# Kernel tuning notes

Measured on AMD Instinct MI355X. Metric: run time of the kernel, lower is better.

Reference implementation:

```python
import jax, jax.numpy as jnp
import numpy as np

N_RAYS, N_SAMPLES, HIDDEN, N_VOXELS = 8192, 256, 64, 1000


def setup_inputs() -> dict:
    key = jax.random.key(0)
    ks = jax.random.split(key, 10)
    ray_start = jax.random.normal(ks[0], (N_RAYS, 3), jnp.float32)
    ray_dir = jax.random.normal(ks[1], (N_RAYS, 3), jnp.float32)
    ray_dir = ray_dir / jnp.linalg.norm(ray_dir, axis=-1, keepdims=True)
    # monotonically increasing depths along each ray
    sampled_depth = jnp.sort(jax.random.uniform(ks[2], (N_RAYS, N_SAMPLES), jnp.float32) * 4.0 + 0.5, axis=-1)
    sampled_dists = jax.random.uniform(ks[3], (N_RAYS, N_SAMPLES), jnp.float32) * 0.02 + 1e-3
    sampled_idx = jax.random.randint(ks[4], (N_RAYS, N_SAMPLES), -333, N_VOXELS).astype(jnp.int64)
    W1 = jax.random.normal(ks[5], (3, HIDDEN), jnp.float32) * 0.5
    b1 = jnp.zeros((HIDDEN,), jnp.float32)
    w_sigma = jax.random.normal(ks[6], (HIDDEN,), jnp.float32) * 0.5
    W_rgb = jax.random.normal(ks[7], (HIDDEN, 3), jnp.float32) * 0.5
    W_dir = jax.random.normal(ks[8], (3, 3), jnp.float32) * 0.5
    b_rgb = jnp.zeros((3,), jnp.float32)
    return {"ray_start": ray_start, "ray_dir": ray_dir, "sampled_depth": sampled_depth,
            "sampled_dists": sampled_dists, "sampled_idx": sampled_idx,
            "W1": W1, "b1": b1, "w_sigma": w_sigma, "W_rgb": W_rgb, "W_dir": W_dir, "b_rgb": b_rgb}


def _volume_render(ray_start, ray_dir, sampled_depth, sampled_dists, sampled_idx,
                   W1, b1, w_sigma, W_rgb, W_dir, b_rgb):
    # sampled_xyz = ray(ray_start, ray_dir, depth)
    xyz = ray_start[:, None, :] + ray_dir[:, None, :] * sampled_depth[..., None]  # [N,P,3]
    h = jax.nn.relu(jnp.einsum('npi,ih->nph', xyz, W1) + b1)                      # [N,P,H]
    sigma = jnp.einsum('nph,h->np', h, w_sigma)                                   # [N,P]
    rgb = jax.nn.sigmoid(jnp.einsum('nph,hc->npc', h, W_rgb)
                         + jnp.einsum('ni,ic->nc', ray_dir, W_dir)[:, None, :] + b_rgb)  # [N,P,3]
    mask = (sampled_idx != -1).astype(sigma.dtype)                                # [N,P]
    # free_energy = relu(sigma) * dists * 7.0, scattered back with zeros at misses
    free_energy = jax.nn.relu(sigma) * sampled_dists * 7.0 * mask
    shifted = jnp.concatenate([jnp.zeros_like(free_energy[:, :1]), free_energy[:, :-1]], axis=-1)
    a = 1.0 - jnp.exp(-free_energy)
    b = jnp.exp(-jnp.cumsum(shifted, axis=-1))
    probs = a * b                                                                 # [N,P]
    depths = jnp.sum(sampled_depth * probs, axis=-1)                              # [N]
    missed = 1.0 - jnp.sum(probs, axis=-1)                                        # [N]
    colors = jnp.sum(rgb * probs[..., None], axis=-2)                             # [N,3]
    return jnp.concatenate([colors, depths[:, None], missed[:, None], probs], axis=-1)  # [N, 3+1+1+P]


def reference(ray_start, ray_dir, sampled_depth, sampled_dists, sampled_idx,
              W1, b1, w_sigma, W_rgb, W_dir, b_rgb):
    return _volume_render(ray_start, ray_dir, sampled_depth, sampled_dists, sampled_idx,
                          W1, b1, w_sigma, W_rgb, W_dir, b_rgb)
```

## Files before the change

kernel.cpp:

```cpp
#include <hip/hip_runtime.h>

#define NRAYS 8192
#define NS    256
#define HID   64
#define NPAIR 32
#define RPB   8
#define SPT   8

typedef _Float16 f16x2 __attribute__((ext_vector_type(2)));

static __device__ __forceinline__ float fdot2(f16x2 a, f16x2 b, float c) {
    return __builtin_amdgcn_fdot2(a, b, c, false);
}
static __device__ __forceinline__ f16x2 mk2(float a, float b) {
    f16x2 v; v.x = (_Float16)a; v.y = (_Float16)b; return v;
}

struct __align__(16) W4  { f16x2 ws, wr, wg, wb; };
struct __align__(8)  AB2 { f16x2 A, B; };

__global__ __launch_bounds__(256) void vr_kernel(
    const float* __restrict__ ray_start,
    const float* __restrict__ ray_dir,
    const float* __restrict__ sampled_depth,
    const float* __restrict__ sampled_dists,
    const int*   __restrict__ sampled_idx,
    const float* __restrict__ W1,
    const float* __restrict__ b1,
    const float* __restrict__ w_sigma,
    const float* __restrict__ W_rgb,
    const float* __restrict__ W_dir,
    const float* __restrict__ b_rgb,
    float* __restrict__ out)
{
    __shared__ W4  sW[NPAIR];
    __shared__ AB2 sAB[RPB][NPAIR];

    const int t = threadIdx.x;
    if (t < NPAIR) {
        const int h0 = 2*t, h1 = 2*t + 1;
        W4 w;
        w.ws = mk2(w_sigma[h0],    w_sigma[h1]);
        w.wr = mk2(W_rgb[h0*3+0],  W_rgb[h1*3+0]);
        w.wg = mk2(W_rgb[h0*3+1],  W_rgb[h1*3+1]);
        w.wb = mk2(W_rgb[h0*3+2],  W_rgb[h1*3+2]);
        sW[t] = w;
    }
    {
        const int rr  = t >> 5;
        const int k   = t & (NPAIR - 1);
        const int ray = blockIdx.x * RPB + rr;
        const float ox = ray_start[ray*3+0], oy = ray_start[ray*3+1], oz = ray_start[ray*3+2];
        const float dx = ray_dir[ray*3+0],  dy = ray_dir[ray*3+1],  dz = ray_dir[ray*3+2];
        const int h0 = 2*k, h1 = 2*k + 1;
        const float u0 = W1[h0], u1 = W1[HID + h0], u2 = W1[2*HID + h0];
        const float v0 = W1[h1], v1 = W1[HID + h1], v2 = W1[2*HID + h1];
        const float A0 = fmaf(u0, ox, fmaf(u1, oy, fmaf(u2, oz, b1[h0])));
        const float B0 = fmaf(u0, dx, fmaf(u1, dy, u2 * dz));
        const float A1 = fmaf(v0, ox, fmaf(v1, oy, fmaf(v2, oz, b1[h1])));
        const float B1 = fmaf(v0, dx, fmaf(v1, dy, v2 * dz));
        AB2 e; e.A = mk2(A0, A1); e.B = mk2(B0, B1);
        sAB[rr][k] = e;
    }
    __syncthreads();

    const int lane = t & 63;
    const int wave = t >> 6;
    const int hl   = lane & 31;
    const int r    = wave * 2 + (lane >> 5);
    const int ray  = blockIdx.x * RPB + r;

    const float dx = ray_dir[ray*3+0], dy = ray_dir[ray*3+1], dz = ray_dir[ray*3+2];
    const float dwr = fmaf(dx, W_dir[0], fmaf(dy, W_dir[3], fmaf(dz, W_dir[6], b_rgb[0])));
    const float dwg = fmaf(dx, W_dir[1], fmaf(dy, W_dir[4], fmaf(dz, W_dir[7], b_rgb[1])));
    const float dwb = fmaf(dx, W_dir[2], fmaf(dy, W_dir[5], fmaf(dz, W_dir[8], b_rgb[2])));

    const size_t rbase = (size_t)ray * NS + (size_t)hl * SPT;
    const float4 dep0 = ((const float4*)(sampled_depth + rbase))[0];
    const float4 dep1 = ((const float4*)(sampled_depth + rbase))[1];
    const float4 dst0 = ((const float4*)(sampled_dists + rbase))[0];
    const float4 dst1 = ((const float4*)(sampled_dists + rbase))[1];
    const int4   vi0  = ((const int4*)(sampled_idx + rbase))[0];
    const int4   vi1  = ((const int4*)(sampled_idx + rbase))[1];

    const float dpt[SPT] = {dep0.x, dep0.y, dep0.z, dep0.w, dep1.x, dep1.y, dep1.z, dep1.w};
    const float dsv[SPT] = {dst0.x, dst0.y, dst0.z, dst0.w, dst1.x, dst1.y, dst1.z, dst1.w};
    const int   vid[SPT] = {vi0.x, vi0.y, vi0.z, vi0.w, vi1.x, vi1.y, vi1.z, vi1.w};

    f16x2 d2[SPT];
#pragma unroll
    for (int j = 0; j < SPT; ++j) d2[j] = mk2(dpt[j], dpt[j]);
    const f16x2 zero2 = mk2(0.f, 0.f);

    float sig[SPT] = {0,0,0,0,0,0,0,0};
    float cr[SPT]  = {0,0,0,0,0,0,0,0};
    float cg[SPT]  = {0,0,0,0,0,0,0,0};
    float cb[SPT]  = {0,0,0,0,0,0,0,0};

#pragma unroll 4
    for (int k = 0; k < NPAIR; ++k) {
        const W4  w  = sW[k];
        const AB2 ab = sAB[r][k];
#pragma unroll
        for (int j = 0; j < SPT; ++j) {
            f16x2 hv = __builtin_elementwise_fma(ab.B, d2[j], ab.A);
            hv = __builtin_elementwise_max(hv, zero2);
            sig[j] = fdot2(hv, w.ws, sig[j]);
            cr[j]  = fdot2(hv, w.wr, cr[j]);
            cg[j]  = fdot2(hv, w.wg, cg[j]);
            cb[j]  = fdot2(hv, w.wb, cb[j]);
        }
    }

    float c[SPT];
    float run = 0.f;
#pragma unroll
    for (int j = 0; j < SPT; ++j) {
        float f = fmaxf(sig[j], 0.f) * dsv[j] * 7.0f;
        if (vid[j] == -1) f = 0.f;
        run += f;
        c[j] = run;
    }

    float tot = run;
#pragma unroll
    for (int off = 1; off < 32; off <<= 1) {
        const float v = __shfl_up(tot, off, 32);
        if (hl >= off) tot += v;
    }
    const float base = tot - run;

    float Eprev = __expf(-base);
    float prob[SPT];
    float s0 = 0.f, s1 = 0.f, s2 = 0.f, s3 = 0.f, s4 = 0.f;
#pragma unroll
    for (int j = 0; j < SPT; ++j) {
        const float Ej = __expf(-(base + c[j]));
        const float p  = Eprev - Ej;
        Eprev = Ej;
        prob[j] = p;
        const float rr = __builtin_amdgcn_rcpf(1.f + __expf(-(cr[j] + dwr)));
        const float gg = __builtin_amdgcn_rcpf(1.f + __expf(-(cg[j] + dwg)));
        const float bb = __builtin_amdgcn_rcpf(1.f + __expf(-(cb[j] + dwb)));
        s0 += p;
        s1 = fmaf(dpt[j], p, s1);
        s2 = fmaf(rr, p, s2);
        s3 = fmaf(gg, p, s3);
        s4 = fmaf(bb, p, s4);
    }

#pragma unroll
    for (int off = 16; off >= 1; off >>= 1) {
        s0 += __shfl_xor(s0, off, 32);
        s1 += __shfl_xor(s1, off, 32);
        s2 += __shfl_xor(s2, off, 32);
        s3 += __shfl_xor(s3, off, 32);
        s4 += __shfl_xor(s4, off, 32);
    }

    float* orow = out + (size_t)ray * (NS + 5);
#pragma unroll
    for (int j = 0; j < SPT; ++j)
        orow[5 + SPT*hl + j] = prob[j];

    if (hl == 0) {
        orow[0] = s2;
        orow[1] = s3;
        orow[2] = s4;
        orow[3] = s1;
        orow[4] = 1.f - s0;
    }
}

extern "C" void kernel_launch(void* const* d_in, const int* in_sizes, int n_in,
                              void* d_out, int out_size, void* d_ws, size_t ws_size,
                              hipStream_t stream)
{
    vr_kernel<<<NRAYS / RPB, 256, 0, stream>>>(
        (const float*)d_in[0],
        (const float*)d_in[1],
        (const float*)d_in[2],
        (const float*)d_in[3],
        (const int*)  d_in[4],
        (const float*)d_in[5],
        (const float*)d_in[6],
        (const float*)d_in[7],
        (const float*)d_in[8],
        (const float*)d_in[9],
        (const float*)d_in[10],
        (float*)d_out);
}
```

Measured before the change: 104.0 us.

## Map one ray per wave with four samples per lane

Each wave of 64 lanes now handles one ray, with four samples per lane, where before each half-wave handled a ray at eight samples per lane. Blocks hold four rays and the launch bound asks for eight blocks per CU. The per-ray hidden-layer coefficients are packed four units at a time into 16-byte shared entries, so each iteration does one shared load of A/B and two of weights. The aim is lower register pressure, higher occupancy and more threads overall. The cost is twice as many weight loads from shared memory per sample and longer 64-wide scan and reduction shuffle chains.

```diff
diff --git a/kernel.cpp b/kernel.cpp
--- a/kernel.cpp
+++ b/kernel.cpp
@@ -4,8 +4,9 @@
 #define NS    256
 #define HID   64
 #define NPAIR 32
-#define RPB   8
-#define SPT   8
+#define NP4   16
+#define RPB   4
+#define SPT   4
 
 typedef _Float16 f16x2 __attribute__((ext_vector_type(2)));
 
@@ -17,9 +18,9 @@
 }
 
 struct __align__(16) W4  { f16x2 ws, wr, wg, wb; };
-struct __align__(8)  AB2 { f16x2 A, B; };
+struct __align__(16) AB4 { f16x2 A01, B01, A23, B23; };
 
-__global__ __launch_bounds__(256) void vr_kernel(
+__global__ __launch_bounds__(256, 8) void vr_kernel(
     const float* __restrict__ ray_start,
     const float* __restrict__ ray_dir,
     const float* __restrict__ sampled_depth,
@@ -34,7 +35,7 @@
     float* __restrict__ out)
 {
     __shared__ W4  sW[NPAIR];
-    __shared__ AB2 sAB[RPB][NPAIR];
+    __shared__ AB4 sAB[RPB][NP4];
 
     const int t = threadIdx.x;
     if (t < NPAIR) {
@@ -47,68 +48,68 @@
         sW[t] = w;
     }
     {
-        const int rr  = t >> 5;
-        const int k   = t & (NPAIR - 1);
+        const int rr  = t >> 6;
+        const int h   = t & 63;
         const int ray = blockIdx.x * RPB + rr;
         const float ox = ray_start[ray*3+0], oy = ray_start[ray*3+1], oz = ray_start[ray*3+2];
         const float dx = ray_dir[ray*3+0],  dy = ray_dir[ray*3+1],  dz = ray_dir[ray*3+2];
-        const int h0 = 2*k, h1 = 2*k + 1;
-        const float u0 = W1[h0], u1 = W1[HID + h0], u2 = W1[2*HID + h0];
-        const float v0 = W1[h1], v1 = W1[HID + h1], v2 = W1[2*HID + h1];
-        const float A0 = fmaf(u0, ox, fmaf(u1, oy, fmaf(u2, oz, b1[h0])));
-        const float B0 = fmaf(u0, dx, fmaf(u1, dy, u2 * dz));
-        const float A1 = fmaf(v0, ox, fmaf(v1, oy, fmaf(v2, oz, b1[h1])));
-        const float B1 = fmaf(v0, dx, fmaf(v1, dy, v2 * dz));
-        AB2 e; e.A = mk2(A0, A1); e.B = mk2(B0, B1);
-        sAB[rr][k] = e;
+        const float w0 = W1[h], w1 = W1[HID + h], w2 = W1[2*HID + h];
+        const float A = fmaf(w0, ox, fmaf(w1, oy, fmaf(w2, oz, b1[h])));
+        const float B = fmaf(w0, dx, fmaf(w1, dy, w2 * dz));
+        const int i = h >> 2, m = h & 3;
+        _Float16* dst16 = (_Float16*)&sAB[rr][i];
+        dst16[(m >> 1) * 4 + (m & 1)]     = (_Float16)A;
+        dst16[(m >> 1) * 4 + (m & 1) + 2] = (_Float16)B;
     }
     __syncthreads();
 
     const int lane = t & 63;
-    const int wave = t >> 6;
-    const int hl   = lane & 31;
-    const int r    = wave * 2 + (lane >> 5);
-    const int ray  = blockIdx.x * RPB + r;
+    const int wv   = t >> 6;
+    const int ray  = blockIdx.x * RPB + wv;
 
     const float dx = ray_dir[ray*3+0], dy = ray_dir[ray*3+1], dz = ray_dir[ray*3+2];
     const float dwr = fmaf(dx, W_dir[0], fmaf(dy, W_dir[3], fmaf(dz, W_dir[6], b_rgb[0])));
     const float dwg = fmaf(dx, W_dir[1], fmaf(dy, W_dir[4], fmaf(dz, W_dir[7], b_rgb[1])));
     const float dwb = fmaf(dx, W_dir[2], fmaf(dy, W_dir[5], fmaf(dz, W_dir[8], b_rgb[2])));
 
-    const size_t rbase = (size_t)ray * NS + (size_t)hl * SPT;
-    const float4 dep0 = ((const float4*)(sampled_depth + rbase))[0];
-    const float4 dep1 = ((const float4*)(sampled_depth + rbase))[1];
-    const float4 dst0 = ((const float4*)(sampled_dists + rbase))[0];
-    const float4 dst1 = ((const float4*)(sampled_dists + rbase))[1];
-    const int4   vi0  = ((const int4*)(sampled_idx + rbase))[0];
-    const int4   vi1  = ((const int4*)(sampled_idx + rbase))[1];
+    const size_t rbase = (size_t)ray * NS + (size_t)lane * SPT;
+    const float4 dep = *(const float4*)(sampled_depth + rbase);
+    const float4 dst = *(const float4*)(sampled_dists + rbase);
+    const int4  vidx = *(const int4*)(sampled_idx + rbase);
 
-    const float dpt[SPT] = {dep0.x, dep0.y, dep0.z, dep0.w, dep1.x, dep1.y, dep1.z, dep1.w};
-    const float dsv[SPT] = {dst0.x, dst0.y, dst0.z, dst0.w, dst1.x, dst1.y, dst1.z, dst1.w};
-    const int   vid[SPT] = {vi0.x, vi0.y, vi0.z, vi0.w, vi1.x, vi1.y, vi1.z, vi1.w};
+    const float dpt[SPT] = {dep.x, dep.y, dep.z, dep.w};
+    const float dsv[SPT] = {dst.x, dst.y, dst.z, dst.w};
+    const int   vid[SPT] = {vidx.x, vidx.y, vidx.z, vidx.w};
 
     f16x2 d2[SPT];
 #pragma unroll
     for (int j = 0; j < SPT; ++j) d2[j] = mk2(dpt[j], dpt[j]);
     const f16x2 zero2 = mk2(0.f, 0.f);
 
-    float sig[SPT] = {0,0,0,0,0,0,0,0};
-    float cr[SPT]  = {0,0,0,0,0,0,0,0};
-    float cg[SPT]  = {0,0,0,0,0,0,0,0};
-    float cb[SPT]  = {0,0,0,0,0,0,0,0};
+    float sig[SPT] = {0,0,0,0};
+    float cr[SPT]  = {0,0,0,0};
+    float cg[SPT]  = {0,0,0,0};
+    float cb[SPT]  = {0,0,0,0};
 
-#pragma unroll 4
-    for (int k = 0; k < NPAIR; ++k) {
-        const W4  w  = sW[k];
-        const AB2 ab = sAB[r][k];
+#pragma unroll 2
+    for (int i = 0; i < NP4; ++i) {
+        const W4  w0 = sW[2*i];
+        const W4  w1 = sW[2*i + 1];
+        const AB4 ab = sAB[wv][i];
 #pragma unroll
         for (int j = 0; j < SPT; ++j) {
-            f16x2 hv = __builtin_elementwise_fma(ab.B, d2[j], ab.A);
-            hv = __builtin_elementwise_max(hv, zero2);
-            sig[j] = fdot2(hv, w.ws, sig[j]);
-            cr[j]  = fdot2(hv, w.wr, cr[j]);
-            cg[j]  = fdot2(hv, w.wg, cg[j]);
-            cb[j]  = fdot2(hv, w.wb, cb[j]);
+            f16x2 hv0 = __builtin_elementwise_fma(ab.B01, d2[j], ab.A01);
+            f16x2 hv1 = __builtin_elementwise_fma(ab.B23, d2[j], ab.A23);
+            hv0 = __builtin_elementwise_max(hv0, zero2);
+            hv1 = __builtin_elementwise_max(hv1, zero2);
+            sig[j] = fdot2(hv0, w0.ws, sig[j]);
+            cr[j]  = fdot2(hv0, w0.wr, cr[j]);
+            cg[j]  = fdot2(hv0, w0.wg, cg[j]);
+            cb[j]  = fdot2(hv0, w0.wb, cb[j]);
+            sig[j] = fdot2(hv1, w1.ws, sig[j]);
+            cr[j]  = fdot2(hv1, w1.wr, cr[j]);
+            cg[j]  = fdot2(hv1, w1.wg, cg[j]);
+            cb[j]  = fdot2(hv1, w1.wb, cb[j]);
         }
     }
 
@@ -124,9 +125,9 @@
 
     float tot = run;
 #pragma unroll
-    for (int off = 1; off < 32; off <<= 1) {
-        const float v = __shfl_up(tot, off, 32);
-        if (hl >= off) tot += v;
+    for (int off = 1; off < 64; off <<= 1) {
+        const float v = __shfl_up(tot, off, 64);
+        if (lane >= off) tot += v;
     }
     const float base = tot - run;
 
@@ -150,20 +151,20 @@
     }
 
 #pragma unroll
-    for (int off = 16; off >= 1; off >>= 1) {
-        s0 += __shfl_xor(s0, off, 32);
-        s1 += __shfl_xor(s1, off, 32);
-        s2 += __shfl_xor(s2, off, 32);
-        s3 += __shfl_xor(s3, off, 32);
-        s4 += __shfl_xor(s4, off, 32);
+    for (int off = 32; off >= 1; off >>= 1) {
+        s0 += __shfl_xor(s0, off, 64);
+        s1 += __shfl_xor(s1, off, 64);
+        s2 += __shfl_xor(s2, off, 64);
+        s3 += __shfl_xor(s3, off, 64);
+        s4 += __shfl_xor(s4, off, 64);
     }
 
     float* orow = out + (size_t)ray * (NS + 5);
 #pragma unroll
     for (int j = 0; j < SPT; ++j)
-        orow[5 + SPT*hl + j] = prob[j];
+        orow[5 + SPT*lane + j] = prob[j];
 
-    if (hl == 0) {
+    if (lane == 0) {
         orow[0] = s2;
         orow[1] = s3;
         orow[2] = s4;
```

Result: slower. 108.2 us (+4.0%).
